# Kernel optimization log

Measured on AMD Instinct MI355X. Metric: run time of the kernel, lower is better.

## Reference

```python
import jax, jax.numpy as jnp
import numpy as np

H, D = 8, 64  # num_attn_head, out_dim
NU, NI = 50000, 50000
E = 100000


def setup_inputs() -> dict:
    key = jax.random.key(0)
    ks = jax.random.split(key, 32)
    def w(k, shape, scale=0.02):
        return jax.random.normal(k, shape, dtype=jnp.float32) * scale
    inp = {
        'x_user': jax.random.normal(ks[0], (NU, 256), dtype=jnp.float32),
        'x_item': jax.random.normal(ks[1], (NI, 256), dtype=jnp.float32),
        'Wq_user': w(ks[2], (512, 256)), 'bq_user': jnp.zeros((512,), jnp.float32),
        'Wk_user': w(ks[3], (512, 256)), 'bk_user': jnp.zeros((512,), jnp.float32),
        'Wv_user': w(ks[4], (512, 256)), 'bv_user': jnp.zeros((512,), jnp.float32),
        'Wq_item': w(ks[5], (512, 256)), 'bq_item': jnp.zeros((512,), jnp.float32),
        'Wk_item': w(ks[6], (512, 256)), 'bk_item': jnp.zeros((512,), jnp.float32),
        'Wv_item': w(ks[7], (512, 256)), 'bv_item': jnp.zeros((512,), jnp.float32),
        'wa_user': w(ks[8], (64,), 0.1), 'wa_item': w(ks[9], (64,), 0.1),
        'src_clicks': jax.random.randint(ks[10], (E,), 0, NU, dtype=jnp.int32),
        'dst_clicks': jax.random.randint(ks[11], (E,), 0, NI, dtype=jnp.int32),
        'src_clicked_by': jax.random.randint(ks[12], (E,), 0, NI, dtype=jnp.int32),
        'dst_clicked_by': jax.random.randint(ks[13], (E,), 0, NU, dtype=jnp.int32),
        'src_follows': jax.random.randint(ks[14], (E,), 0, NU, dtype=jnp.int32),
        'dst_follows': jax.random.randint(ks[15], (E,), 0, NU, dtype=jnp.int32),
    }
    return inp


def _proj(x, W, b):
    # torch Linear: y = x @ W.T + b, then view(-1, H, D)
    return (x @ W.T + b).reshape(x.shape[0], H, D)


def _etype_agg(aq_dst, ak_src, v_src, src, dst, num_dst):
    # edge score per head: (key_attn[src] + query_attn[dst]) / sqrt(D)
    score = (ak_src[src] + aq_dst[dst]) * (1.0 / np.sqrt(D))  # [E,H]
    m = jax.ops.segment_max(score, dst, num_segments=num_dst)  # [Nd,H]
    ex = jnp.exp(score - m[dst])
    den = jax.ops.segment_sum(ex, dst, num_segments=num_dst)
    attn = ex / den[dst]  # edge_softmax over incoming edges per dst, per head
    msg = v_src[src] * attn[:, :, None]  # [E,H,D]
    s = jax.ops.segment_sum(msg, dst, num_segments=num_dst)  # [Nd,H,D]
    deg = jax.ops.segment_sum(jnp.ones((src.shape[0],), jnp.float32), dst,
                              num_segments=num_dst)  # [Nd]
    return s / jnp.maximum(deg, 1.0)[:, None, None]  # inner agg = mean


def reference(x_user, x_item,
              Wq_user, bq_user, Wk_user, bk_user, Wv_user, bv_user,
              Wq_item, bq_item, Wk_item, bk_item, Wv_item, bv_item,
              wa_user, wa_item,
              src_clicks, dst_clicks, src_clicked_by, dst_clicked_by,
              src_follows, dst_follows):
    q_u = _proj(x_user, Wq_user, bq_user)
    k_u = _proj(x_user, Wk_user, bk_user)
    v_u = _proj(x_user, Wv_user, bv_user)
    q_i = _proj(x_item, Wq_item, bq_item)
    k_i = _proj(x_item, Wk_item, bk_item)
    v_i = _proj(x_item, Wv_item, bv_item)
    # node_attn_weight: Linear(D, 1, bias=False) per ntype -> scalar per head
    aq_u = jnp.einsum('nhd,d->nh', q_u, wa_user)
    ak_u = jnp.einsum('nhd,d->nh', k_u, wa_user)
    aq_i = jnp.einsum('nhd,d->nh', q_i, wa_item)
    ak_i = jnp.einsum('nhd,d->nh', k_i, wa_item)
    nu, ni = x_user.shape[0], x_item.shape[0]
    # ('user','clicks','item'): src=user, dst=item
    h_item = _etype_agg(aq_i, ak_u, v_u, src_clicks, dst_clicks, ni)
    # ('item','clicked_by','user'): src=item, dst=user
    h_u1 = _etype_agg(aq_u, ak_i, v_i, src_clicked_by, dst_clicked_by, nu)
    # ('user','follows','user'): src=user, dst=user
    h_u2 = _etype_agg(aq_u, ak_u, v_u, src_follows, dst_follows, nu)
    h_user = h_u1 + h_u2  # inter-type agg = sum
    return (h_user.reshape(nu, H * D), h_item.reshape(ni, H * D))
```

## Files before the change

kernel.cpp:

```cpp
#include <hip/hip_runtime.h>

#define NUSER 50000
#define NITEM 50000
#define NEDGE 100000
#define HDIM  512
#define KIN   256

typedef unsigned short ushort_t;
typedef __attribute__((ext_vector_type(8))) short short8;
typedef __attribute__((ext_vector_type(4))) float f32x4;

static __device__ __forceinline__ float bf2f(ushort_t u) {
    unsigned v = ((unsigned)u) << 16;
    float f;
    __builtin_memcpy(&f, &v, 4);
    return f;
}
static __device__ __forceinline__ ushort_t f2bf(float f) {
    unsigned u;
    __builtin_memcpy(&u, &f, 4);
    unsigned r = u + 0x7fffu + ((u >> 16) & 1u);
    return (ushort_t)(r >> 16);
}
static __device__ __forceinline__ float ldf(const void* p, long i, bool fp32) {
    return fp32 ? ((const float*)p)[i] : bf2f(((const ushort_t*)p)[i]);
}

__global__ void detect_kernel(const ushort_t* __restrict__ x, int* __restrict__ flag) {
    __shared__ float red[256];
    int tid = threadIdx.x;
    float m = 0.f;
    for (int i = tid; i < 4096; i += 256) m = fmaxf(m, fabsf(bf2f(x[i])));
    red[tid] = m;
    __syncthreads();
    for (int s = 128; s > 0; s >>= 1) {
        if (tid < s) red[tid] = fmaxf(red[tid], red[tid + s]);
        __syncthreads();
    }
    if (tid == 0) *flag = (red[0] > 1e6f) ? 1 : 0;
}

__global__ void eff_w_all_kernel(
        const void* __restrict__ Wqu, const void* __restrict__ bqu,
        const void* __restrict__ Wku, const void* __restrict__ bku,
        const void* __restrict__ Wqi, const void* __restrict__ bqi,
        const void* __restrict__ Wki, const void* __restrict__ bki,
        const void* __restrict__ wau, const void* __restrict__ wai,
        float* __restrict__ weffu, float* __restrict__ weffi,
        float* __restrict__ beffu, float* __restrict__ beffi,
        const int* __restrict__ flag) {
    int y = blockIdx.y;
    const void* W  = (y == 0) ? Wqu : (y == 1) ? Wku : (y == 2) ? Wqi : Wki;
    const void* b  = (y == 0) ? bqu : (y == 1) ? bku : (y == 2) ? bqi : bki;
    const void* wa = (y < 2) ? wau : wai;
    float* weff = ((y < 2) ? weffu : weffi) + (y & 1) * 2048;
    float* beff = ((y < 2) ? beffu : beffi) + (y & 1) * 8;
    bool fp32 = (*flag != 0);
    int h = blockIdx.x;
    int k = threadIdx.x;
    __shared__ float was[64];
    __shared__ float red[64];
    if (k < 64) was[k] = ldf(wa, k, fp32);
    __syncthreads();
    float s = 0.f;
#pragma unroll 8
    for (int d = 0; d < 64; d++)
        s += was[d] * ldf(W, (long)(h * 64 + d) * KIN + k, fp32);
    weff[h * KIN + k] = 0.125f * s;
    if (k < 64) red[k] = was[k] * ldf(b, h * 64 + k, fp32);
    __syncthreads();
    if (k == 0) {
        float t = 0.f;
        for (int d = 0; d < 64; d++) t += red[d];
        beff[h] = 0.125f * t;
    }
}

static __device__ __forceinline__ void stage_tile_fp32(
        const float* __restrict__ G, ushort_t* lds, int base_row, int maxrow, int tid) {
    int lane = tid & 63, w = tid >> 6;
#pragma unroll
    for (int i = 0; i < 16; i++) {
        int row_l = i * 4 + w;
        int grow = base_row + row_l; if (grow > maxrow) grow = maxrow;
        float4 v = *(const float4*)(G + (size_t)grow * KIN + lane * 4);
        uint2 u;
        u.x = (unsigned)f2bf(v.x) | ((unsigned)f2bf(v.y) << 16);
        u.y = (unsigned)f2bf(v.z) | ((unsigned)f2bf(v.w) << 16);
        int byte = row_l * 512 + ((lane * 8 + ((row_l & 7) << 6)) & 511);
        *(uint2*)((char*)lds + byte) = u;
    }
}
static __device__ __forceinline__ void stage_tile_bf16(
        const ushort_t* __restrict__ G, ushort_t* lds, int base_row, int maxrow, int tid) {
#pragma unroll
    for (int i = 0; i < 8; i++) {
        int chunk = i * 256 + tid;
        int row_l = chunk >> 5, hw = chunk & 31;
        int grow = base_row + row_l; if (grow > maxrow) grow = maxrow;
        uint4 v = *(const uint4*)(G + (size_t)grow * KIN + hw * 8);
        int byte = row_l * 512 + ((hw * 16 + ((row_l & 7) << 6)) & 511);
        *(uint4*)((char*)lds + byte) = v;
    }
}
static __device__ __forceinline__ short8 frag_read(const ushort_t* lds, int row_l,
                                                   int ks, int rq) {
    int byte = row_l * 512 + (((ks * 64 + rq * 16) + ((row_l & 7) << 6)) & 511);
    return *(const short8*)((const char*)lds + byte);
}

__global__ __launch_bounds__(256, 2) void gemm_v5_kernel(
        const void* __restrict__ Au, const void* __restrict__ Wu,
        const void* __restrict__ bu, ushort_t* __restrict__ Cu,
        const void* __restrict__ Ai, const void* __restrict__ Wi,
        const void* __restrict__ bi, ushort_t* __restrict__ Ci,
        int M, const int* __restrict__ flag) {
    __shared__ __align__(16) ushort_t As[64 * 256];
    __shared__ __align__(16) ushort_t Bs[64 * 256];
    __shared__ __align__(16) ushort_t ep[4][2048];
    const void* A    = blockIdx.y ? Ai : Au;
    const void* W    = blockIdx.y ? Wi : Wu;
    const void* bias = blockIdx.y ? bi : bu;
    ushort_t* C      = blockIdx.y ? Ci : Cu;
    bool fp32 = (*flag != 0);
    int tid = threadIdx.x, lane = tid & 63, w = tid >> 6;
    int b = blockIdx.x, cg = b & 1, rc0 = b >> 1;
    int colq = lane & 15, rq = lane >> 4;
    int nf0 = cg * 16 + w * 4;

    if (fp32) stage_tile_fp32((const float*)A, As, rc0 * 64, M - 1, tid);
    else      stage_tile_bf16((const ushort_t*)A, As, rc0 * 64, M - 1, tid);

    short8 breg[4][8];
#pragma unroll
    for (int q = 0; q < 4; q++) {
        if (fp32) stage_tile_fp32((const float*)W, Bs, cg * 256 + q * 64, 511, tid);
        else      stage_tile_bf16((const ushort_t*)W, Bs, cg * 256 + q * 64, 511, tid);
        __syncthreads();
        if (w == q) {
#pragma unroll
            for (int nf = 0; nf < 4; nf++)
#pragma unroll
                for (int ks = 0; ks < 8; ks++)
                    breg[nf][ks] = frag_read(Bs, nf * 16 + colq, ks, rq);
        }
        __syncthreads();
    }
    float bv[4];
#pragma unroll
    for (int nf = 0; nf < 4; nf++)
        bv[nf] = ldf(bias, (nf0 + nf) * 16 + colq, fp32);

    bool first = true;
    for (int rc = rc0; rc < 782; rc += 256) {
        if (!first) {
            __syncthreads();
            if (fp32) stage_tile_fp32((const float*)A, As, rc * 64, M - 1, tid);
            else      stage_tile_bf16((const ushort_t*)A, As, rc * 64, M - 1, tid);
            __syncthreads();
        }
        first = false;
#pragma unroll
        for (int rt = 0; rt < 2; rt++) {
            f32x4 acc[2][4] = {};
#pragma unroll
            for (int ks = 0; ks < 8; ks++) {
                short8 a0 = frag_read(As, rt * 32 + colq, ks, rq);
                short8 a1 = frag_read(As, rt * 32 + 16 + colq, ks, rq);
#pragma unroll
                for (int nf = 0; nf < 4; nf++) {
                    acc[0][nf] = __builtin_amdgcn_mfma_f32_16x16x32_bf16(a0, breg[nf][ks], acc[0][nf], 0, 0, 0);
                    acc[1][nf] = __builtin_amdgcn_mfma_f32_16x16x32_bf16(a1, breg[nf][ks], acc[1][nf], 0, 0, 0);
                }
            }
            char* epb = (char*)&ep[w][0];
            int rot = rq * 32;
#pragma unroll
            for (int mi = 0; mi < 2; mi++)
#pragma unroll
                for (int r = 0; r < 4; r++) {
                    int row = mi * 16 + rq * 4 + r;
#pragma unroll
                    for (int nf = 0; nf < 4; nf++)
                        *(ushort_t*)(epb + row * 128 + ((nf * 32 + colq * 2 + rot) & 127)) =
                            f2bf(acc[mi][nf][r] + bv[nf]);
                }
#pragma unroll
            for (int j = 0; j < 4; j++) {
                int idx = j * 64 + lane;
                int rl = idx >> 3, cb8 = idx & 7;
                int grow = rc * 64 + rt * 32 + rl;
                if (grow < M)
                    *(uint4*)(C + (size_t)grow * HDIM + cg * 256 + w * 64 + cb8 * 8) =
                        *(const uint4*)(epb + rl * 128 + ((cb8 * 16 + ((rl >> 2) & 3) * 32) & 127));
            }
        }
    }
}

__global__ void attn_all_kernel(const void* __restrict__ xu, const void* __restrict__ xi,
                                const float* __restrict__ weffu, const float* __restrict__ weffi,
                                const float* __restrict__ beffu, const float* __restrict__ beffi,
                                float* __restrict__ aqu, float* __restrict__ aku,
                                float* __restrict__ aqi, float* __restrict__ aki,
                                const int* __restrict__ flag) {
    const void* X = blockIdx.y ? xi : xu;
    const float* weff = blockIdx.y ? weffi : weffu;
    const float* beff = blockIdx.y ? beffi : beffu;
    float* aq = blockIdx.y ? aqi : aqu;
    float* ak = blockIdx.y ? aki : aku;
    __shared__ float wl[16 * KIN];
    int tid = threadIdx.x;
    for (int i = tid; i < 16 * KIN; i += 256) wl[i] = weff[i];
    bool fp32 = (*flag != 0);
    __syncthreads();
    int lane = tid & 63, w = tid >> 6;
    for (int g = blockIdx.x; g < 12500; g += 1024) {
        int n = g * 4 + w;
        float xv0, xv1, xv2, xv3;
        if (fp32) {
            const float* xr = (const float*)X + (size_t)n * KIN + lane * 4;
            float4 u = *(const float4*)xr;
            xv0 = u.x; xv1 = u.y; xv2 = u.z; xv3 = u.w;
        } else {
            const ushort_t* xr = (const ushort_t*)X + (size_t)n * KIN + lane * 4;
            uint2 u = *(const uint2*)xr;
            xv0 = bf2f(u.x & 0xffff); xv1 = bf2f(u.x >> 16);
            xv2 = bf2f(u.y & 0xffff); xv3 = bf2f(u.y >> 16);
        }
        float p[16];
#pragma unroll
        for (int o = 0; o < 16; o++) {
            float4 wv = *(const float4*)&wl[o * KIN + lane * 4];
            p[o] = xv0 * wv.x + xv1 * wv.y + xv2 * wv.z + xv3 * wv.w;
        }
#pragma unroll
        for (int o = 0; o < 16; o++) {
            float v = p[o];
#pragma unroll
            for (int m = 32; m > 0; m >>= 1) v += __shfl_xor(v, m);
            if (lane == o) {
                float r = v + beff[o];
                if (o < 8) aq[n * 8 + o] = r;
                else       ak[n * 8 + (o - 8)] = r;
            }
        }
    }
}

__global__ void edge_pass1_all_kernel(
        const int* __restrict__ s0, const int* __restrict__ d0,
        const float* __restrict__ ak0, const float* __restrict__ aq0,
        float* __restrict__ w0, float* __restrict__ den_0, int* __restrict__ deg_0,
        const int* __restrict__ s1, const int* __restrict__ d1,
        const float* __restrict__ ak1, const float* __restrict__ aq1,
        float* __restrict__ w1, float* __restrict__ den_1, int* __restrict__ deg_1,
        const int* __restrict__ s2, const int* __restrict__ d2,
        const float* __restrict__ ak2, const float* __restrict__ aq2,
        float* __restrict__ w2, float* __restrict__ den_2, int* __restrict__ deg_2) {
    int y = blockIdx.y;
    const int* src = (y == 0) ? s0 : (y == 1) ? s1 : s2;
    const int* dst = (y == 0) ? d0 : (y == 1) ? d1 : d2;
    const float* ak = (y == 0) ? ak0 : (y == 1) ? ak1 : ak2;
    const float* aq = (y == 0) ? aq0 : (y == 1) ? aq1 : aq2;
    float* wbuf = (y == 0) ? w0 : (y == 1) ? w1 : w2;
    float* den  = (y == 0) ? den_0 : (y == 1) ? den_1 : den_2;
    int* deg    = (y == 0) ? deg_0 : (y == 1) ? deg_1 : deg_2;
    int e = blockIdx.x * 256 + threadIdx.x;
    if (e >= NEDGE) return;
    int s = src[e], d = dst[e];
#pragma unroll
    for (int h = 0; h < 8; h++) {
        float sc = ak[s * 8 + h] + aq[d * 8 + h];
        float wv = __expf(sc);
        wbuf[e * 8 + h] = wv;
        atomicAdd(&den[d * 8 + h], wv);
    }
    atomicAdd(&deg[d], 1);
}

__global__ void scan3_kernel(const int* __restrict__ deg0, const int* __restrict__ deg1,
                             const int* __restrict__ deg2, int* __restrict__ offs0,
                             int* __restrict__ offs1, int* __restrict__ offs2) {
    const int Nd = NUSER;
    const int* deg = blockIdx.x == 0 ? deg0 : (blockIdx.x == 1 ? deg1 : deg2);
    int* offs = blockIdx.x == 0 ? offs0 : (blockIdx.x == 1 ? offs1 : offs2);
    __shared__ int lds[1024];
    int tid = threadIdx.x;
    int chunk = (Nd + 1023) >> 10;
    int s = tid * chunk;
    int e = s + chunk; if (e > Nd) e = Nd;
    int local = 0;
    for (int i = s; i < e; i++) local += deg[i];
    lds[tid] = local;
    __syncthreads();
    for (int d = 1; d < 1024; d <<= 1) {
        int v = (tid >= d) ? lds[tid - d] : 0;
        __syncthreads();
        lds[tid] += v;
        __syncthreads();
    }
    int run = (tid > 0) ? lds[tid - 1] : 0;
    for (int i = s; i < e; i++) { offs[i] = run; run += deg[i]; }
}

__global__ void edge_scatter_all_kernel(
        const int* __restrict__ d0, const int* __restrict__ o0,
        int* __restrict__ c0, int* __restrict__ e0,
        const int* __restrict__ d1, const int* __restrict__ o1,
        int* __restrict__ c1, int* __restrict__ e1,
        const int* __restrict__ d2, const int* __restrict__ o2,
        int* __restrict__ c2, int* __restrict__ e2) {
    int y = blockIdx.y;
    const int* dst = (y == 0) ? d0 : (y == 1) ? d1 : d2;
    const int* offs = (y == 0) ? o0 : (y == 1) ? o1 : o2;
    int* cur = (y == 0) ? c0 : (y == 1) ? c1 : c2;
    int* esort = (y == 0) ? e0 : (y == 1) ? e1 : e2;
    int e = blockIdx.x * 256 + threadIdx.x;
    if (e >= NEDGE) return;
    int d = dst[e];
    int p = offs[d] + atomicAdd(&cur[d], 1);
    esort[p] = e;
}

static __device__ __forceinline__ void wave_agg_etype(
        int d, int lane, int hh,
        const int* __restrict__ src, const int* __restrict__ es,
        const int* __restrict__ offs, const int* __restrict__ deg,
        const float* __restrict__ den, const float* __restrict__ wbuf,
        const ushort_t* __restrict__ V, float* acc , int* dg_out) {
    int dg = deg[d];
    int o0 = offs[d];
    *dg_out = dg;
    for (int base = 0; base < dg; base += 64) {
        int idx = base + lane;
        int ci = idx < dg ? idx : dg - 1;
        int el = es[o0 + ci];
        int sl = src[el];
        int kmax = dg - base; if (kmax > 64) kmax = 64;
        for (int k = 0; k < kmax; k++) {
            int e = __shfl(el, k);
            int s = __shfl(sl, k);
            float wv = wbuf[e * 8 + hh];
            uint4 vv = *(const uint4*)(V + (size_t)s * HDIM + lane * 8);
            acc[0] += bf2f(vv.x & 0xffff) * wv;
            acc[1] += bf2f(vv.x >> 16) * wv;
            acc[2] += bf2f(vv.y & 0xffff) * wv;
            acc[3] += bf2f(vv.y >> 16) * wv;
            acc[4] += bf2f(vv.z & 0xffff) * wv;
            acc[5] += bf2f(vv.z >> 16) * wv;
            acc[6] += bf2f(vv.w & 0xffff) * wv;
            acc[7] += bf2f(vv.w >> 16) * wv;
        }
    }
}

__global__ void agg_all_kernel(
        const int* __restrict__ src0, const int* __restrict__ es0,
        const int* __restrict__ offs0, const int* __restrict__ deg0,
        const float* __restrict__ den0, const float* __restrict__ wb0,
        const ushort_t* __restrict__ V0,
        const int* __restrict__ src1, const int* __restrict__ es1,
        const int* __restrict__ offs1, const int* __restrict__ deg1,
        const float* __restrict__ den1, const float* __restrict__ wb1,
        const ushort_t* __restrict__ V1,
        const int* __restrict__ src2, const int* __restrict__ es2,
        const int* __restrict__ offs2, const int* __restrict__ deg2,
        const float* __restrict__ den2, const float* __restrict__ wb2,
        const ushort_t* __restrict__ V2,
        void* __restrict__ outv, const int* __restrict__ flag) {
    int lane = threadIdx.x & 63;
    int wv = threadIdx.x >> 6;
    int hh = lane >> 3;
    bool f32o = (*flag != 0);
    for (int wid = blockIdx.x; wid < 25000; wid += 2048) {
        if (wid < 12500) {
            int d = wid * 4 + wv;
            float acc[8] = {};
            int dg;
            wave_agg_etype(d, lane, hh, src0, es0, offs0, deg0, den0, wb0, V0, acc, &dg);
            float inv = dg > 0 ? 1.0f / (den0[d * 8 + hh] * (float)dg) : 0.f;
            size_t base = (size_t)NUSER * HDIM + (size_t)d * HDIM + lane * 8;
            if (f32o) {
                float* o = (float*)outv + base;
#pragma unroll
                for (int j = 0; j < 8; j++) o[j] = acc[j] * inv;
            } else {
                uint4 o;
                o.x = (unsigned)f2bf(acc[0] * inv) | ((unsigned)f2bf(acc[1] * inv) << 16);
                o.y = (unsigned)f2bf(acc[2] * inv) | ((unsigned)f2bf(acc[3] * inv) << 16);
                o.z = (unsigned)f2bf(acc[4] * inv) | ((unsigned)f2bf(acc[5] * inv) << 16);
                o.w = (unsigned)f2bf(acc[6] * inv) | ((unsigned)f2bf(acc[7] * inv) << 16);
                *(uint4*)((ushort_t*)outv + base) = o;
            }
        } else {
            int d = (wid - 12500) * 4 + wv;
            float acc1[8] = {}, acc2[8] = {};
            int dg1, dg2;
            wave_agg_etype(d, lane, hh, src1, es1, offs1, deg1, den1, wb1, V1, acc1, &dg1);
            wave_agg_etype(d, lane, hh, src2, es2, offs2, deg2, den2, wb2, V2, acc2, &dg2);
            float inv1 = dg1 > 0 ? 1.0f / (den1[d * 8 + hh] * (float)dg1) : 0.f;
            float inv2 = dg2 > 0 ? 1.0f / (den2[d * 8 + hh] * (float)dg2) : 0.f;
            float r[8];
#pragma unroll
            for (int j = 0; j < 8; j++) r[j] = acc1[j] * inv1 + acc2[j] * inv2;
            size_t base = (size_t)d * HDIM + lane * 8;
            if (f32o) {
                float* o = (float*)outv + base;
#pragma unroll
                for (int j = 0; j < 8; j++) o[j] = r[j];
            } else {
                uint4 o;
                o.x = (unsigned)f2bf(r[0]) | ((unsigned)f2bf(r[1]) << 16);
                o.y = (unsigned)f2bf(r[2]) | ((unsigned)f2bf(r[3]) << 16);
                o.z = (unsigned)f2bf(r[4]) | ((unsigned)f2bf(r[5]) << 16);
                o.w = (unsigned)f2bf(r[6]) | ((unsigned)f2bf(r[7]) << 16);
                *(uint4*)((ushort_t*)outv + base) = o;
            }
        }
    }
}

extern "C" void kernel_launch(void* const* d_in, const int* in_sizes, int n_in,
                              void* d_out, int out_size, void* d_ws, size_t ws_size,
                              hipStream_t stream) {
    const void* x_user  = d_in[0];
    const void* x_item  = d_in[1];
    const void* Wq_user = d_in[2];
    const void* bq_user = d_in[3];
    const void* Wk_user = d_in[4];
    const void* bk_user = d_in[5];
    const void* Wv_user = d_in[6];
    const void* bv_user = d_in[7];
    const void* Wq_item = d_in[8];
    const void* bq_item = d_in[9];
    const void* Wk_item = d_in[10];
    const void* bk_item = d_in[11];
    const void* Wv_item = d_in[12];
    const void* bv_item = d_in[13];
    const void* wa_user = d_in[14];
    const void* wa_item = d_in[15];
    const int* src_clicks     = (const int*)d_in[16];
    const int* dst_clicks     = (const int*)d_in[17];
    const int* src_clicked_by = (const int*)d_in[18];
    const int* dst_clicked_by = (const int*)d_in[19];
    const int* src_follows    = (const int*)d_in[20];
    const int* dst_follows    = (const int*)d_in[21];

    char* ws = (char*)d_ws;
    ushort_t* v_u  = (ushort_t*)(ws + 0);
    ushort_t* v_i  = (ushort_t*)(ws + 51200000);
    float* aq_u    = (float*)(ws + 102400000);
    float* ak_u    = (float*)(ws + 104000000);
    float* aq_i    = (float*)(ws + 105600000);
    float* ak_i    = (float*)(ws + 107200000);
    float* weff_u  = (float*)(ws + 108800000);
    float* weff_i  = (float*)(ws + 108816384);
    float* beff_u  = (float*)(ws + 108832768);
    float* beff_i  = (float*)(ws + 108832832);
    int*   dflag   = (int*)(ws + 108832896);
    const size_t Z = 108832960;
    float* den0 = (float*)(ws + Z + 0);
    float* den1 = (float*)(ws + Z + 1600000);
    float* den2 = (float*)(ws + Z + 3200000);
    int* deg0   = (int*)(ws + Z + 4800000);
    int* deg1   = (int*)(ws + Z + 5000000);
    int* deg2   = (int*)(ws + Z + 5200000);
    int* cur0   = (int*)(ws + Z + 5400000);
    int* cur1   = (int*)(ws + Z + 5600000);
    int* cur2   = (int*)(ws + Z + 5800000);
    const size_t ZLEN = 6000000;
    int* offs0  = (int*)(ws + Z + 6000000);
    int* offs1  = (int*)(ws + Z + 6200000);
    int* offs2  = (int*)(ws + Z + 6400000);
    int* es0    = (int*)(ws + Z + 6600000);
    int* es1    = (int*)(ws + Z + 7000000);
    int* es2    = (int*)(ws + Z + 7400000);
    float* wb0  = (float*)(ws + Z + 7800000);
    float* wb1  = (float*)(ws + Z + 11000000);
    float* wb2  = (float*)(ws + Z + 14200000);
    if (ws_size < Z + 17400000) return;

    detect_kernel<<<1, 256, 0, stream>>>((const ushort_t*)x_user, dflag);

    hipMemsetAsync(ws + Z, 0, ZLEN, stream);

    eff_w_all_kernel<<<dim3(8, 4), 256, 0, stream>>>(
        Wq_user, bq_user, Wk_user, bk_user, Wq_item, bq_item, Wk_item, bk_item,
        wa_user, wa_item, weff_u, weff_i, beff_u, beff_i, dflag);

    gemm_v5_kernel<<<dim3(512, 2), 256, 0, stream>>>(
        x_user, Wv_user, bv_user, v_u, x_item, Wv_item, bv_item, v_i, NUSER, dflag);

    attn_all_kernel<<<dim3(1024, 2), 256, 0, stream>>>(
        x_user, x_item, weff_u, weff_i, beff_u, beff_i,
        aq_u, ak_u, aq_i, ak_i, dflag);

    edge_pass1_all_kernel<<<dim3(391, 3), 256, 0, stream>>>(
        src_clicks, dst_clicks, ak_u, aq_i, wb0, den0, deg0,
        src_clicked_by, dst_clicked_by, ak_i, aq_u, wb1, den1, deg1,
        src_follows, dst_follows, ak_u, aq_u, wb2, den2, deg2);

    scan3_kernel<<<3, 1024, 0, stream>>>(deg0, deg1, deg2, offs0, offs1, offs2);

    edge_scatter_all_kernel<<<dim3(391, 3), 256, 0, stream>>>(
        dst_clicks, offs0, cur0, es0,
        dst_clicked_by, offs1, cur1, es1,
        dst_follows, offs2, cur2, es2);

    agg_all_kernel<<<2048, 256, 0, stream>>>(
        src_clicks, es0, offs0, deg0, den0, wb0, v_u,
        src_clicked_by, es1, offs1, deg1, den1, wb1, v_i,
        src_follows, es2, offs2, deg2, den2, wb2, v_u,
        d_out, dflag);
}
```

Baseline: 836.5 us.

## Fuse edge score exp and softmax denominator into aggregation pass

Removes the per-edge pass that computed exp scores, stored them to a weight buffer and atomically accumulated per-destination denominators. The aggregation wave now computes exp(ak[src]+aq[dst]) on the fly and sums the denominator locally in registers, so only degree counting remains as a separate pass. This drops the 3x100k x8 atomics, the weight-buffer writes and reads, and a larger memset. In exchange it adds redundant exp computation per lane inside the inner loop.

Result: faster. 702.1 us (-16.1%).

```diff
diff --git a/kernel.cpp b/kernel.cpp
--- a/kernel.cpp
+++ b/kernel.cpp
@@ -248,35 +248,16 @@
     }
 }
 
-__global__ void edge_pass1_all_kernel(
-        const int* __restrict__ s0, const int* __restrict__ d0,
-        const float* __restrict__ ak0, const float* __restrict__ aq0,
-        float* __restrict__ w0, float* __restrict__ den_0, int* __restrict__ deg_0,
-        const int* __restrict__ s1, const int* __restrict__ d1,
-        const float* __restrict__ ak1, const float* __restrict__ aq1,
-        float* __restrict__ w1, float* __restrict__ den_1, int* __restrict__ deg_1,
-        const int* __restrict__ s2, const int* __restrict__ d2,
-        const float* __restrict__ ak2, const float* __restrict__ aq2,
-        float* __restrict__ w2, float* __restrict__ den_2, int* __restrict__ deg_2) {
+__global__ void deg_count_all_kernel(
+        const int* __restrict__ d0, int* __restrict__ deg_0,
+        const int* __restrict__ d1, int* __restrict__ deg_1,
+        const int* __restrict__ d2, int* __restrict__ deg_2) {
     int y = blockIdx.y;
-    const int* src = (y == 0) ? s0 : (y == 1) ? s1 : s2;
     const int* dst = (y == 0) ? d0 : (y == 1) ? d1 : d2;
-    const float* ak = (y == 0) ? ak0 : (y == 1) ? ak1 : ak2;
-    const float* aq = (y == 0) ? aq0 : (y == 1) ? aq1 : aq2;
-    float* wbuf = (y == 0) ? w0 : (y == 1) ? w1 : w2;
-    float* den  = (y == 0) ? den_0 : (y == 1) ? den_1 : den_2;
-    int* deg    = (y == 0) ? deg_0 : (y == 1) ? deg_1 : deg_2;
+    int* deg       = (y == 0) ? deg_0 : (y == 1) ? deg_1 : deg_2;
     int e = blockIdx.x * 256 + threadIdx.x;
     if (e >= NEDGE) return;
-    int s = src[e], d = dst[e];
-#pragma unroll
-    for (int h = 0; h < 8; h++) {
-        float sc = ak[s * 8 + h] + aq[d * 8 + h];
-        float wv = __expf(sc);
-        wbuf[e * 8 + h] = wv;
-        atomicAdd(&den[d * 8 + h], wv);
-    }
-    atomicAdd(&deg[d], 1);
+    atomicAdd(&deg[dst[e]], 1);
 }
 
 __global__ void scan3_kernel(const int* __restrict__ deg0, const int* __restrict__ deg1,
@@ -327,11 +308,14 @@
         int d, int lane, int hh,
         const int* __restrict__ src, const int* __restrict__ es,
         const int* __restrict__ offs, const int* __restrict__ deg,
-        const float* __restrict__ den, const float* __restrict__ wbuf,
-        const ushort_t* __restrict__ V, float* acc , int* dg_out) {
+        const float* __restrict__ ak, const float* __restrict__ aq,
+        const ushort_t* __restrict__ V, float* acc ,
+        float* den_out, int* dg_out) {
     int dg = deg[d];
     int o0 = offs[d];
     *dg_out = dg;
+    float aqv = aq[d * 8 + hh];
+    float den = 0.f;
     for (int base = 0; base < dg; base += 64) {
         int idx = base + lane;
         int ci = idx < dg ? idx : dg - 1;
@@ -339,9 +323,9 @@
         int sl = src[el];
         int kmax = dg - base; if (kmax > 64) kmax = 64;
         for (int k = 0; k < kmax; k++) {
-            int e = __shfl(el, k);
             int s = __shfl(sl, k);
-            float wv = wbuf[e * 8 + hh];
+            float wv = __expf(ak[s * 8 + hh] + aqv);
+            den += wv;
             uint4 vv = *(const uint4*)(V + (size_t)s * HDIM + lane * 8);
             acc[0] += bf2f(vv.x & 0xffff) * wv;
             acc[1] += bf2f(vv.x >> 16) * wv;
@@ -353,21 +337,21 @@
             acc[7] += bf2f(vv.w >> 16) * wv;
         }
     }
+    *den_out = den;
 }
 
 __global__ void agg_all_kernel(
         const int* __restrict__ src0, const int* __restrict__ es0,
         const int* __restrict__ offs0, const int* __restrict__ deg0,
-        const float* __restrict__ den0, const float* __restrict__ wb0,
         const ushort_t* __restrict__ V0,
         const int* __restrict__ src1, const int* __restrict__ es1,
         const int* __restrict__ offs1, const int* __restrict__ deg1,
-        const float* __restrict__ den1, const float* __restrict__ wb1,
         const ushort_t* __restrict__ V1,
         const int* __restrict__ src2, const int* __restrict__ es2,
         const int* __restrict__ offs2, const int* __restrict__ deg2,
-        const float* __restrict__ den2, const float* __restrict__ wb2,
         const ushort_t* __restrict__ V2,
+        const float* __restrict__ aq_u, const float* __restrict__ ak_u,
+        const float* __restrict__ aq_i, const float* __restrict__ ak_i,
         void* __restrict__ outv, const int* __restrict__ flag) {
     int lane = threadIdx.x & 63;
     int wv = threadIdx.x >> 6;
@@ -377,9 +361,9 @@
         if (wid < 12500) {
             int d = wid * 4 + wv;
             float acc[8] = {};
-            int dg;
-            wave_agg_etype(d, lane, hh, src0, es0, offs0, deg0, den0, wb0, V0, acc, &dg);
-            float inv = dg > 0 ? 1.0f / (den0[d * 8 + hh] * (float)dg) : 0.f;
+            float den; int dg;
+            wave_agg_etype(d, lane, hh, src0, es0, offs0, deg0, ak_u, aq_i, V0, acc, &den, &dg);
+            float inv = dg > 0 ? 1.0f / (den * (float)dg) : 0.f;
             size_t base = (size_t)NUSER * HDIM + (size_t)d * HDIM + lane * 8;
             if (f32o) {
                 float* o = (float*)outv + base;
@@ -396,11 +380,11 @@
         } else {
             int d = (wid - 12500) * 4 + wv;
             float acc1[8] = {}, acc2[8] = {};
-            int dg1, dg2;
-            wave_agg_etype(d, lane, hh, src1, es1, offs1, deg1, den1, wb1, V1, acc1, &dg1);
-            wave_agg_etype(d, lane, hh, src2, es2, offs2, deg2, den2, wb2, V2, acc2, &dg2);
-            float inv1 = dg1 > 0 ? 1.0f / (den1[d * 8 + hh] * (float)dg1) : 0.f;
-            float inv2 = dg2 > 0 ? 1.0f / (den2[d * 8 + hh] * (float)dg2) : 0.f;
+            float den1, den2; int dg1, dg2;
+            wave_agg_etype(d, lane, hh, src1, es1, offs1, deg1, ak_i, aq_u, V1, acc1, &den1, &dg1);
+            wave_agg_etype(d, lane, hh, src2, es2, offs2, deg2, ak_u, aq_u, V2, acc2, &den2, &dg2);
+            float inv1 = dg1 > 0 ? 1.0f / (den1 * (float)dg1) : 0.f;
+            float inv2 = dg2 > 0 ? 1.0f / (den2 * (float)dg2) : 0.f;
             float r[8];
 #pragma unroll
             for (int j = 0; j < 8; j++) r[j] = acc1[j] * inv1 + acc2[j] * inv2;
@@ -460,30 +444,23 @@
     float* beff_i  = (float*)(ws + 108832832);
     int*   dflag   = (int*)(ws + 108832896);
     const size_t Z = 108832960;
-    float* den0 = (float*)(ws + Z + 0);
-    float* den1 = (float*)(ws + Z + 1600000);
-    float* den2 = (float*)(ws + Z + 3200000);
     int* deg0   = (int*)(ws + Z + 4800000);
     int* deg1   = (int*)(ws + Z + 5000000);
     int* deg2   = (int*)(ws + Z + 5200000);
     int* cur0   = (int*)(ws + Z + 5400000);
     int* cur1   = (int*)(ws + Z + 5600000);
     int* cur2   = (int*)(ws + Z + 5800000);
-    const size_t ZLEN = 6000000;
     int* offs0  = (int*)(ws + Z + 6000000);
     int* offs1  = (int*)(ws + Z + 6200000);
     int* offs2  = (int*)(ws + Z + 6400000);
     int* es0    = (int*)(ws + Z + 6600000);
     int* es1    = (int*)(ws + Z + 7000000);
     int* es2    = (int*)(ws + Z + 7400000);
-    float* wb0  = (float*)(ws + Z + 7800000);
-    float* wb1  = (float*)(ws + Z + 11000000);
-    float* wb2  = (float*)(ws + Z + 14200000);
     if (ws_size < Z + 17400000) return;
 
     detect_kernel<<<1, 256, 0, stream>>>((const ushort_t*)x_user, dflag);
 
-    hipMemsetAsync(ws + Z, 0, ZLEN, stream);
+    hipMemsetAsync(ws + Z + 4800000, 0, 1200000, stream);
 
     eff_w_all_kernel<<<dim3(8, 4), 256, 0, stream>>>(
         Wq_user, bq_user, Wk_user, bk_user, Wq_item, bq_item, Wk_item, bk_item,
@@ -496,10 +473,8 @@
         x_user, x_item, weff_u, weff_i, beff_u, beff_i,
         aq_u, ak_u, aq_i, ak_i, dflag);
 
-    edge_pass1_all_kernel<<<dim3(391, 3), 256, 0, stream>>>(
-        src_clicks, dst_clicks, ak_u, aq_i, wb0, den0, deg0,
-        src_clicked_by, dst_clicked_by, ak_i, aq_u, wb1, den1, deg1,
-        src_follows, dst_follows, ak_u, aq_u, wb2, den2, deg2);
+    deg_count_all_kernel<<<dim3(391, 3), 256, 0, stream>>>(
+        dst_clicks, deg0, dst_clicked_by, deg1, dst_follows, deg2);
 
     scan3_kernel<<<3, 1024, 0, stream>>>(deg0, deg1, deg2, offs0, offs1, offs2);
 
@@ -509,8 +484,9 @@
         dst_follows, offs2, cur2, es2);
 
     agg_all_kernel<<<2048, 256, 0, stream>>>(
-        src_clicks, es0, offs0, deg0, den0, wb0, v_u,
-        src_clicked_by, es1, offs1, deg1, den1, wb1, v_i,
-        src_follows, es2, offs2, deg2, den2, wb2, v_u,
+        src_clicks, es0, offs0, deg0, v_u,
+        src_clicked_by, es1, offs1, deg1, v_i,
+        src_follows, es2, offs2, deg2, v_u,
+        aq_u, ak_u, aq_i, ak_i,
         d_out, dflag);
 }
```
